# Performance work log

Measured on AMD Instinct MI355X. Metric: run time of the kernel, lower is better.

The kernel has to match this reference:

```python
import jax, jax.numpy as jnp
import numpy as np

L, H, D, DH, DFF, V, P, T, R = 12, 12, 768, 64, 3072, 30522, 512, 2, 50
RAT_LAYER = 6  # original condition: 5 < idx < 7


def layer_norm(x, g, b, eps=1e-12):
    m = x.mean(-1, keepdims=True)
    v = ((x - m) ** 2).mean(-1, keepdims=True)
    return (x - m) / jnp.sqrt(v + eps) * g + b


def setup_inputs() -> dict:
    key = jax.random.key(0)
    ks = iter(jax.random.split(key, 20))
    def n(shape, s=0.02):
        return jax.random.normal(next(ks), shape, dtype=jnp.float32) * s
    inp = dict(
        input_ids=jax.random.randint(next(ks), (4, 512), 0, V, dtype=jnp.int32),
        relations=jax.random.randint(next(ks), (4, 512, 512), 0, R, dtype=jnp.int32),
        attention_mask=jnp.ones((4, 512), dtype=jnp.int32),
        word_emb=n((V, D)), pos_emb=n((P, D)), type_emb=n((T, D)),
        emb_ln_g=jnp.ones((D,)), emb_ln_b=jnp.zeros((D,)),
        Wq=n((L, D, D)), bq=jnp.zeros((L, D)), Wk=n((L, D, D)), bk=jnp.zeros((L, D)),
        Wv=n((L, D, D)), bv=jnp.zeros((L, D)), Wo=n((L, D, D)), bo=jnp.zeros((L, D)),
        ln1_g=jnp.ones((L, D)), ln1_b=jnp.zeros((L, D)),
        Wi=n((L, D, DFF)), bi=jnp.zeros((L, DFF)),
        Wf=n((L, DFF, D)), bf=jnp.zeros((L, D)),
        ln2_g=jnp.ones((L, D)), ln2_b=jnp.zeros((L, D)),
        key_rel=n((L, R, DH)), val_rel=n((L, R, DH)),
        pool_w=n((D, D)), pool_b=jnp.zeros((D,)),
    )
    return inp


def reference(input_ids, relations, attention_mask, word_emb, pos_emb, type_emb,
              emb_ln_g, emb_ln_b, Wq, bq, Wk, bk, Wv, bv, Wo, bo, ln1_g, ln1_b,
              Wi, bi, Wf, bf, ln2_g, ln2_b, key_rel, val_rel, pool_w, pool_b):
    B, S = input_ids.shape
    # BERT embeddings (token_type_ids = zeros as in module default)
    h = word_emb[input_ids] + pos_emb[jnp.arange(S)][None] + type_emb[0][None, None]
    h = layer_norm(h, emb_ln_g, emb_ln_b)
    ext_mask = (1.0 - attention_mask.astype(jnp.float32))[:, None, None, :] * -10000.0
    inv_sqrt_dh = np.float32(1.0 / np.sqrt(DH))
    for i in range(L):
        q = (h @ Wq[i] + bq[i]).reshape(B, S, H, DH).transpose(0, 2, 1, 3)
        k = (h @ Wk[i] + bk[i]).reshape(B, S, H, DH).transpose(0, 2, 1, 3)
        v = (h @ Wv[i] + bv[i]).reshape(B, S, H, DH).transpose(0, 2, 1, 3)
        scores = jnp.einsum('bhsd,bhtd->bhst', q, k)
        if i == RAT_LAYER:
            kr = key_rel[i][relations]            # [B,S,S,DH] gathered relation keys
            scores = scores + jnp.einsum('bhsd,bstd->bhst', q, kr)
        scores = scores * inv_sqrt_dh + ext_mask
        probs = jax.nn.softmax(scores, axis=-1)   # dropout = identity (eval)
        ctx = jnp.einsum('bhst,bhtd->bhsd', probs, v)
        if i == RAT_LAYER:
            vr = val_rel[i][relations]            # [B,S,S,DH] gathered relation values
            ctx = ctx + jnp.einsum('bhst,bstd->bhsd', probs, vr)
        ctx = ctx.transpose(0, 2, 1, 3).reshape(B, S, D)
        attn_out = layer_norm(ctx @ Wo[i] + bo[i] + h, ln1_g[i], ln1_b[i])
        ff = jax.nn.gelu(attn_out @ Wi[i] + bi[i], approximate=False)
        h = layer_norm(ff @ Wf[i] + bf[i] + attn_out, ln2_g[i], ln2_b[i])
    pooled = jnp.tanh(h[:, 0] @ pool_w + pool_b)
    return h, pooled
```

## Files before the change

kernel.cpp:

```cpp
#include <hip/hip_runtime.h>
#include <math.h>

typedef unsigned short u16;
typedef unsigned int   u32;
typedef __bf16  bf16x8 __attribute__((ext_vector_type(8)));
typedef float   f32x4  __attribute__((ext_vector_type(4)));
typedef u16     u16x8  __attribute__((ext_vector_type(8)));

__device__ __forceinline__ u16 f2bf(float f) {
  u32 u = __builtin_bit_cast(u32, f);
  u32 r = (u + 0x7fffu + ((u >> 16) & 1u)) >> 16;
  return (u16)r;
}
__device__ __forceinline__ float bf2f(u16 h) {
  u32 u = ((u32)h) << 16;
  return __builtin_bit_cast(float, u);
}
__device__ __forceinline__ void gload16(const void* g, void* l) {
  __builtin_amdgcn_global_load_lds((const __attribute__((address_space(1))) void*)g,
                                   (__attribute__((address_space(3))) void*)l, 16, 0, 0);
}
__device__ __forceinline__ bf16x8 ld_bf8(const u16* p) {
  u16x8 v = *(const u16x8*)p;
  return __builtin_bit_cast(bf16x8, v);
}
__device__ __forceinline__ f32x4 mfma16(bf16x8 a, bf16x8 b, f32x4 c) {
  return __builtin_amdgcn_mfma_f32_16x16x32_bf16(a, b, c, 0, 0, 0);
}

struct ConvP {
  const float *wq, *wk, *wv, *wo, *wi, *wf;
  u16 *oqkv, *oo, *oi, *of;
};
__global__ __launch_bounds__(256) void conv_weights(ConvP p) {
  int t = blockIdx.x;
  const float* in; u16* out; int K, N, tn, tk;
  if (t < 1728) { int wh = t / 576, tt = t % 576;
    in = wh==0 ? p.wq : (wh==1 ? p.wk : p.wv);
    out = p.oqkv + (size_t)wh * 768 * 768;
    K = 768; N = 768; tn = tt % 24; tk = tt / 24;
  } else if (t < 2304) { int tt = t - 1728; in = p.wo; out = p.oo; K=768;  N=768;  tn=tt%24; tk=tt/24; }
  else if (t < 4608)   { int tt = t - 2304; in = p.wi; out = p.oi; K=768;  N=3072; tn=tt%96; tk=tt/96; }
  else                 { int tt = t - 4608; in = p.wf; out = p.of; K=3072; N=768;  tn=tt%24; tk=tt/24; }
  int n0 = tn*32, k0 = tk*32;
  __shared__ float tile[32][33];
  int x = threadIdx.x, y = threadIdx.y;
  #pragma unroll
  for (int j = 0; j < 4; ++j)
    tile[y + j*8][x] = in[(size_t)(k0 + y + j*8) * N + n0 + x];
  __syncthreads();
  #pragma unroll
  for (int j = 0; j < 4; ++j)
    out[(size_t)(n0 + y + j*8) * K + k0 + x] = f2bf(tile[x][y + j*8]);
}

struct GP {
  const u16* A; const u16* B;
  int K, N;
  long sA, sB, sOut;
  const float* bias; const float* res;
  float* outF; u16* outB;
  const float* bq; const float* bk; const float* bv;
  u16* qO; u16* kO; u16* vO;
};

template<int BM, int BN, int WAVES, int EPI, int KS>
__global__ __launch_bounds__(WAVES*64) void gemm_bt(GP p) {
  constexpr int THREADS = WAVES * 64;
  constexpr int WC = WAVES / 2;
  constexpr int WM = BM / 2, WN = BN / WC, MR = WM / 16, NR = WN / 16;
  constexpr int AIT = BM * 64 / (THREADS * 8);
  constexpr int BIT = BN * 64 / (THREADS * 8);
  const int tid = threadIdx.x;
  const int wave = tid >> 6, lane = tid & 63;
  const int wr = wave / WC, wc = wave % WC;
  const int wm0 = wr * WM, wn0 = wc * WN;
  const int bn = blockIdx.x, bm = blockIdx.y, bz = blockIdx.z;
  const int K = p.K;
  const int kLen = K / KS;
  const int kBeg = (KS > 1) ? bz * kLen : 0;
  const u16* A  = p.A + ((KS > 1) ? 0 : (size_t)bz * p.sA);
  const u16* Bp = p.B + ((KS > 1) ? 0 : (size_t)bz * p.sB);
  const int rowA0 = bm * BM, colB0 = bn * BN;

  __shared__ __align__(16) u16 lds[(BM + BN) * 64];
  u16* Al = lds; u16* Bl = lds + BM * 64;

  f32x4 acc[MR][NR];
  #pragma unroll
  for (int i = 0; i < MR; ++i)
    #pragma unroll
    for (int j = 0; j < NR; ++j) acc[i][j] = f32x4{0.f,0.f,0.f,0.f};

  for (int kt = kBeg; kt < kBeg + kLen; kt += 64) {
    #pragma unroll
    for (int it = 0; it < AIT; ++it) {
      int e = tid * 8 + it * THREADS * 8;
      gload16(A + (size_t)(rowA0 + (e >> 6)) * K + kt + (e & 63), Al + e);
    }
    #pragma unroll
    for (int it = 0; it < BIT; ++it) {
      int e = tid * 8 + it * THREADS * 8;
      gload16(Bp + (size_t)(colB0 + (e >> 6)) * K + kt + (e & 63), Bl + e);
    }
    __syncthreads();
    #pragma unroll
    for (int ks = 0; ks < 2; ++ks) {
      bf16x8 av[MR]; bf16x8 bw[NR];
      #pragma unroll
      for (int mf = 0; mf < MR; ++mf)
        av[mf] = ld_bf8(Al + (wm0 + mf*16 + (lane&15))*64 + ks*32 + (lane>>4)*8);
      #pragma unroll
      for (int nf = 0; nf < NR; ++nf)
        bw[nf] = ld_bf8(Bl + (wn0 + nf*16 + (lane&15))*64 + ks*32 + (lane>>4)*8);
      #pragma unroll
      for (int mf = 0; mf < MR; ++mf)
        #pragma unroll
        for (int nf = 0; nf < NR; ++nf)
          acc[mf][nf] = mfma16(av[mf], bw[nf], acc[mf][nf]);
    }
    __syncthreads();
  }

  #pragma unroll
  for (int mf = 0; mf < MR; ++mf) {
    #pragma unroll
    for (int nf = 0; nf < NR; ++nf) {
      int col = colB0 + wn0 + nf*16 + (lane & 15);
      #pragma unroll
      for (int reg = 0; reg < 4; ++reg) {
        int row = rowA0 + wm0 + mf*16 + (lane >> 4)*4 + reg;
        float v = acc[mf][nf][reg];
        if constexpr (EPI == 0) {
          int wh = col / 768, cc = col % 768;
          int hh = cc >> 6, d = col & 63;
          int b = row >> 9, s = row & 511;
          const float* bias = wh==0 ? p.bq : (wh==1 ? p.bk : p.bv);
          u16 o = f2bf(v + bias[cc]);
          if (wh == 0)      p.qO[((((size_t)b*12 + hh)*512 + s) << 6) + d] = o;
          else if (wh == 1) p.kO[((((size_t)b*12 + hh)*512 + s) << 6) + d] = o;
          else              p.vO[((((size_t)b*12 + hh)*64  + d) << 9) + s] = o;
        } else if constexpr (EPI == 2) {
          p.outF[(size_t)bz * p.sOut + (size_t)row * p.N + col] = v;
        } else {
          float xg = v + p.bias[col];
          float gg = 0.5f * xg * (1.f + erff(xg * 0.70710678118f));
          p.outB[(size_t)row * p.N + col] = f2bf(gg);
        }
      }
    }
  }
}

template<int RAT>
__global__ __launch_bounds__(512) void flash_attn(
    const u16* __restrict__ q, const u16* __restrict__ k, const u16* __restrict__ v,
    const int* __restrict__ mask, u16* __restrict__ ctx,
    const float* __restrict__ qr, const int* __restrict__ rel,
    float* __restrict__ wbins) {
  const int head = blockIdx.x;
  const int bm = blockIdx.y;
  const int b = head / 12, hh = head % 12;
  const int tid = threadIdx.x, wave = tid >> 6, lane = tid & 63;
  const int wr = wave >> 1, wc = wave & 1;
  const int row0 = bm * 64;
  const u16* qb = q + (size_t)head * 512 * 64;
  const u16* kb = k + (size_t)head * 512 * 64;
  const u16* vb = v + (size_t)head * 64 * 512;

  __shared__ __align__(16) u16 Kl[2][64*64];
  __shared__ __align__(16) u16 Vl[2][64*64];
  __shared__ __align__(16) u16 pw[8][16*72];
  __shared__ float em_lds[512];
  __shared__ float mlb[4][16][2];
  __shared__ float qlds[RAT ? 64 : 1][RAT ? 52 : 1];
  __shared__ float wlds[RAT ? 2 : 1][RAT ? 64 : 1][RAT ? 50 : 1];
  __shared__ float scl[RAT ? 2 : 1][RAT ? 64 : 1];
  __shared__ float aex[RAT ? 64 : 1][RAT ? 3 : 1];

  em_lds[tid] = -10000.f * (1.f - (float)mask[b*512 + tid]);
  if constexpr (RAT) {
    for (int i = tid; i < 2*64*50; i += 512) ((float*)wlds)[i] = 0.f;
    for (int i = tid; i < 64*50; i += 512) {
      int rr = i % 50, sr = i / 50;
      qlds[sr][rr] = qr[((size_t)head*512 + row0 + sr)*50 + rr];
    }
  }

  const int qrow = row0 + wr*16 + (lane & 15);
  bf16x8 qf[2];
  qf[0] = ld_bf8(qb + (size_t)qrow*64 +      (lane>>4)*8);
  qf[1] = ld_bf8(qb + (size_t)qrow*64 + 32 + (lane>>4)*8);
  __syncthreads();

  f32x4 ctxacc[4];
  #pragma unroll
  for (int nf = 0; nf < 4; ++nf) ctxacc[nf] = f32x4{0.f,0.f,0.f,0.f};
  float mrun[4], lrun[4];
  #pragma unroll
  for (int r = 0; r < 4; ++r) { mrun[r] = -3.0e38f; lrun[r] = 0.f; }

  const int g = lane >> 4;
  for (int it = 0; it < 4; ++it) {
    {
      int prow = tid >> 3, lcol = (tid & 7) ^ (prow & 7);
      int t0a = it*64, t0b = 256 + it*64;
      gload16(kb + (size_t)(t0a + prow)*64 + lcol*8, Kl[0] + tid*8);
      gload16(kb + (size_t)(t0b + prow)*64 + lcol*8, Kl[1] + tid*8);
      gload16(vb + (size_t)prow*512 + t0a + lcol*8, Vl[0] + tid*8);
      gload16(vb + (size_t)prow*512 + t0b + lcol*8, Vl[1] + tid*8);
    }
    __syncthreads();
    const int tbase = wc*256 + it*64;

    f32x4 s[4];
    #pragma unroll
    for (int nf = 0; nf < 4; ++nf) s[nf] = f32x4{0.f,0.f,0.f,0.f};
    #pragma unroll
    for (int ks = 0; ks < 2; ++ks)
      #pragma unroll
      for (int nf = 0; nf < 4; ++nf) {
        int row = nf*16 + (lane & 15);
        int c16 = (ks*4 + g) ^ (row & 7);
        bf16x8 kf = ld_bf8(Kl[wc] + row*64 + c16*8);
        s[nf] = mfma16(qf[ks], kf, s[nf]);
      }

    u32 rr4[RAT ? 4 : 1];
    if constexpr (RAT) {
      #pragma unroll
      for (int nf = 0; nf < 4; ++nf) {
        int tt = tbase + nf*16 + (lane & 15);
        u32 pack = 0;
        #pragma unroll
        for (int reg = 0; reg < 4; ++reg) {
          int rl = wr*16 + (lane>>4)*4 + reg;
          int rr = rel[((size_t)(b*512 + row0 + rl))*512 + tt];
          pack |= (u32)rr << (8*reg);
          s[nf][reg] += qlds[rl][rr];
        }
        rr4[nf] = pack;
      }
    }

    float em4[4];
    #pragma unroll
    for (int nf = 0; nf < 4; ++nf) em4[nf] = em_lds[tbase + nf*16 + (lane & 15)];

    float scale_[4];
    #pragma unroll
    for (int reg = 0; reg < 4; ++reg) {
      float pm = -3.0e38f;
      #pragma unroll
      for (int nf = 0; nf < 4; ++nf) {
        s[nf][reg] = s[nf][reg]*0.125f + em4[nf];
        pm = fmaxf(pm, s[nf][reg]);
      }
      #pragma unroll
      for (int o = 1; o < 16; o <<= 1) pm = fmaxf(pm, __shfl_xor(pm, o));
      float mnew = fmaxf(mrun[reg], pm);
      float sc = __expf(mrun[reg] - mnew);
      mrun[reg] = mnew;
      scale_[reg] = sc;
      float lsum = 0.f;
      #pragma unroll
      for (int nf = 0; nf < 4; ++nf) {
        float e = __expf(s[nf][reg] - mnew);
        s[nf][reg] = e;
        lsum += e;
      }
      #pragma unroll
      for (int o = 1; o < 16; o <<= 1) lsum += __shfl_xor(lsum, o);
      lrun[reg] = lrun[reg]*sc + lsum;
      if constexpr (RAT) {
        if ((lane & 15) == 0) scl[wc][wr*16 + (lane>>4)*4 + reg] = sc;
      }
    }

    if constexpr (RAT) {
      for (int i = lane; i < 16*50; i += 64) {
        int r = i / 50;
        wlds[wc][wr*16 + r][i % 50] *= scl[wc][wr*16 + r];
      }
      #pragma unroll
      for (int nf = 0; nf < 4; ++nf)
        #pragma unroll
        for (int reg = 0; reg < 4; ++reg) {
          int rl = wr*16 + (lane>>4)*4 + reg;
          int rr = (rr4[nf] >> (8*reg)) & 255;
          atomicAdd(&wlds[wc][rl][rr], s[nf][reg]);
        }
    }

    #pragma unroll
    for (int nf = 0; nf < 4; ++nf)
      #pragma unroll
      for (int reg = 0; reg < 4; ++reg) {
        int qq = (lane>>4)*4 + reg;
        pw[wave][qq*72 + nf*16 + (lane & 15)] = f2bf(s[nf][reg]);
      }

    #pragma unroll
    for (int nf = 0; nf < 4; ++nf)
      #pragma unroll
      for (int reg = 0; reg < 4; ++reg)
        ctxacc[nf][reg] *= scale_[reg];
    #pragma unroll
    for (int ks = 0; ks < 2; ++ks) {
      bf16x8 pf = ld_bf8(pw[wave] + (lane & 15)*72 + ks*32 + g*8);
      #pragma unroll
      for (int nf = 0; nf < 4; ++nf) {
        int row = nf*16 + (lane & 15);
        int c16 = (ks*4 + g) ^ (row & 7);
        bf16x8 vf = ld_bf8(Vl[wc] + row*64 + c16*8);
        ctxacc[nf] = mfma16(pf, vf, ctxacc[nf]);
      }
    }
    __syncthreads();
  }

  float* mergeF = (float*)pw;
  if (wc == 1) {
    #pragma unroll
    for (int nf = 0; nf < 4; ++nf)
      #pragma unroll
      for (int reg = 0; reg < 4; ++reg)
        mergeF[(wr*16 + (lane>>4)*4 + reg)*66 + nf*16 + (lane & 15)] = ctxacc[nf][reg];
    if ((lane & 15) == 0) {
      #pragma unroll
      for (int reg = 0; reg < 4; ++reg) {
        mlb[wr][(lane>>4)*4 + reg][0] = mrun[reg];
        mlb[wr][(lane>>4)*4 + reg][1] = lrun[reg];
      }
    }
  }
  __syncthreads();
  if (wc == 0) {
    float a1[4], a2[4], linv[4];
    #pragma unroll
    for (int reg = 0; reg < 4; ++reg) {
      int r = (lane>>4)*4 + reg;
      float m2 = mlb[wr][r][0], l2 = mlb[wr][r][1];
      float mn = fmaxf(mrun[reg], m2);
      a1[reg] = __expf(mrun[reg] - mn);
      a2[reg] = __expf(m2 - mn);
      linv[reg] = 1.f / (lrun[reg]*a1[reg] + l2*a2[reg]);
      if constexpr (RAT) {
        if ((lane & 15) == 0) {
          aex[wr*16 + r][0] = a1[reg];
          aex[wr*16 + r][1] = a2[reg];
          aex[wr*16 + r][2] = linv[reg];
        }
      }
    }
    #pragma unroll
    for (int nf = 0; nf < 4; ++nf)
      #pragma unroll
      for (int reg = 0; reg < 4; ++reg) {
        int r = wr*16 + (lane>>4)*4 + reg;
        int qg = row0 + r;
        int d = nf*16 + (lane & 15);
        float v2 = mergeF[r*66 + d];
        ctx[((size_t)(b*512 + qg))*768 + hh*64 + d] =
            f2bf((ctxacc[nf][reg]*a1[reg] + v2*a2[reg]) * linv[reg]);
      }
  }
  if constexpr (RAT) {
    __syncthreads();
    for (int i = tid; i < 64*50; i += 512) {
      int sr = i / 50, rr = i % 50;
      wbins[((size_t)head*512 + row0 + sr)*50 + rr] =
          (wlds[0][sr][rr]*aex[sr][0] + wlds[1][sr][rr]*aex[sr][1]) * aex[sr][2];
    }
  }
}

__global__ __launch_bounds__(256) void rat_qr(const u16* __restrict__ q,
    const float* __restrict__ kr, float* __restrict__ qr) {
  int idx = blockIdx.x * 256 + threadIdx.x;
  if (idx >= 24576 * 50) return;
  int r = idx % 50; size_t bhs = (size_t)idx / 50;
  const u16* qp = q + bhs * 64;
  const float* kp = kr + r * 64;
  float acc = 0.f;
  #pragma unroll
  for (int d = 0; d < 64; ++d) acc += bf2f(qp[d]) * kp[d];
  qr[idx] = acc;
}

__global__ __launch_bounds__(256) void rat_apply(const float* __restrict__ wbins,
    const float* __restrict__ vr, u16* __restrict__ ctx) {
  __shared__ float vrl[50*64];
  __shared__ float wl[32*50];
  int tid = threadIdx.x;
  int rows0 = blockIdx.x * 32;
  for (int i = tid; i < 50*64; i += 256) vrl[i] = vr[i];
  for (int i = tid; i < 32*50; i += 256) wl[i] = wbins[(size_t)rows0*50 + i];
  __syncthreads();
  int wave = tid >> 6, lane = tid & 63;
  #pragma unroll
  for (int i = 0; i < 8; ++i) {
    int r = wave*8 + i;
    size_t idx = (size_t)rows0 + r;
    float acc = 0.f;
    #pragma unroll
    for (int j = 0; j < 50; ++j) acc += wl[r*50 + j] * vrl[j*64 + lane];
    int s = (int)(idx & 511); size_t bh = idx >> 9;
    int b = (int)(bh / 12), hh = (int)(bh % 12);
    u16* cp = ctx + ((size_t)(b*512 + s))*768 + hh*64 + lane;
    *cp = f2bf(bf2f(*cp) + acc);
  }
}

__global__ __launch_bounds__(256) void embed_ln(const int* __restrict__ ids,
    const float* __restrict__ we, const float* __restrict__ pe, const float* __restrict__ te,
    const float* __restrict__ g, const float* __restrict__ b,
    float* __restrict__ hF, u16* __restrict__ hB) {
  int row = blockIdx.x, tid = threadIdx.x;
  int s = row & 511;
  int id = ids[row];
  float x[3];
  #pragma unroll
  for (int j = 0; j < 3; ++j) {
    int d = tid + j*256;
    x[j] = we[(size_t)id*768 + d] + pe[(size_t)s*768 + d] + te[d];
  }
  __shared__ float red[4];
  float sm = x[0] + x[1] + x[2];
  #pragma unroll
  for (int o = 32; o; o >>= 1) sm += __shfl_xor(sm, o);
  if (!(tid & 63)) red[tid >> 6] = sm;
  __syncthreads();
  float mean = (red[0]+red[1]+red[2]+red[3]) * (1.f/768.f);
  __syncthreads();
  float q = 0.f;
  #pragma unroll
  for (int j = 0; j < 3; ++j) { float d = x[j] - mean; q += d*d; }
  #pragma unroll
  for (int o = 32; o; o >>= 1) q += __shfl_xor(q, o);
  if (!(tid & 63)) red[tid >> 6] = q;
  __syncthreads();
  float inv = rsqrtf((red[0]+red[1]+red[2]+red[3]) * (1.f/768.f) + 1e-12f);
  #pragma unroll
  for (int j = 0; j < 3; ++j) {
    int d = tid + j*256;
    float y = (x[j] - mean) * inv * g[d] + b[d];
    hF[(size_t)row*768 + d] = y;
    hB[(size_t)row*768 + d] = f2bf(y);
  }
}

__global__ __launch_bounds__(256) void ln_fused(const float* __restrict__ p0,
    const float* __restrict__ p1, const float* __restrict__ p2, const float* __restrict__ p3,
    int np, const float* __restrict__ bias, const float* __restrict__ res,
    const float* __restrict__ g, const float* __restrict__ b,
    float* __restrict__ oF, u16* __restrict__ oB) {
  int row = blockIdx.x, tid = threadIdx.x;
  size_t base = (size_t)row * 768;
  float v[3];
  #pragma unroll
  for (int j = 0; j < 3; ++j) {
    int d = tid + j*256;
    float x = p0[base + d];
    if (np > 1) x += p1[base + d];
    if (np > 2) x += p2[base + d];
    if (np > 3) x += p3[base + d];
    v[j] = x + bias[d] + res[base + d];
  }
  __shared__ float red[4];
  float sm = v[0] + v[1] + v[2];
  #pragma unroll
  for (int o = 32; o; o >>= 1) sm += __shfl_xor(sm, o);
  if (!(tid & 63)) red[tid >> 6] = sm;
  __syncthreads();
  float mean = (red[0]+red[1]+red[2]+red[3]) * (1.f/768.f);
  __syncthreads();
  float q = 0.f;
  #pragma unroll
  for (int j = 0; j < 3; ++j) { float d = v[j] - mean; q += d*d; }
  #pragma unroll
  for (int o = 32; o; o >>= 1) q += __shfl_xor(q, o);
  if (!(tid & 63)) red[tid >> 6] = q;
  __syncthreads();
  float inv = rsqrtf((red[0]+red[1]+red[2]+red[3]) * (1.f/768.f) + 1e-12f);
  #pragma unroll
  for (int j = 0; j < 3; ++j) {
    int d = tid + j*256;
    float y = (v[j] - mean) * inv * g[d] + b[d];
    oF[base + d] = y;
    oB[base + d] = f2bf(y);
  }
}

__global__ __launch_bounds__(256) void pooler_k(const float* __restrict__ h,
    const float* __restrict__ w, const float* __restrict__ bias, float* __restrict__ out) {
  int b = blockIdx.x, tid = threadIdx.x;
  __shared__ float hr[768];
  for (int i = tid; i < 768; i += 256) hr[i] = h[((size_t)b*512)*768 + i];
  __syncthreads();
  float a0 = 0.f, a1 = 0.f, a2 = 0.f;
  for (int kk = 0; kk < 768; ++kk) {
    float hv = hr[kk];
    const float* wr = w + (size_t)kk*768;
    a0 += hv * wr[tid]; a1 += hv * wr[tid+256]; a2 += hv * wr[tid+512];
  }
  out[(size_t)b*768 + tid]       = tanhf(a0 + bias[tid]);
  out[(size_t)b*768 + tid + 256] = tanhf(a1 + bias[tid+256]);
  out[(size_t)b*768 + tid + 512] = tanhf(a2 + bias[tid+512]);
}

__global__ __launch_bounds__(256) void copy_out(const float* __restrict__ in, float* __restrict__ out) {
  size_t i = ((size_t)blockIdx.x * 256 + threadIdx.x) * 4;
  *(float4*)(out + i) = *(const float4*)(in + i);
}

extern "C" void kernel_launch(void* const* d_in, const int* in_sizes, int n_in,
                              void* d_out, int out_size, void* d_ws, size_t ws_size,
                              hipStream_t stream) {
  const int*   ids   = (const int*)d_in[0];
  const int*   rel   = (const int*)d_in[1];
  const int*   amask = (const int*)d_in[2];
  const float* we    = (const float*)d_in[3];
  const float* pe    = (const float*)d_in[4];
  const float* te    = (const float*)d_in[5];
  const float* eg    = (const float*)d_in[6];
  const float* ebb   = (const float*)d_in[7];
  const float* Wq    = (const float*)d_in[8];
  const float* bq    = (const float*)d_in[9];
  const float* Wk    = (const float*)d_in[10];
  const float* bk    = (const float*)d_in[11];
  const float* Wv    = (const float*)d_in[12];
  const float* bv    = (const float*)d_in[13];
  const float* Wo    = (const float*)d_in[14];
  const float* bo    = (const float*)d_in[15];
  const float* g1    = (const float*)d_in[16];
  const float* b1    = (const float*)d_in[17];
  const float* Wi    = (const float*)d_in[18];
  const float* bi    = (const float*)d_in[19];
  const float* Wf    = (const float*)d_in[20];
  const float* bfp   = (const float*)d_in[21];
  const float* g2    = (const float*)d_in[22];
  const float* b2    = (const float*)d_in[23];
  const float* krel  = (const float*)d_in[24];
  const float* vrel  = (const float*)d_in[25];
  const float* pwp   = (const float*)d_in[26];
  const float* pbp   = (const float*)d_in[27];
  (void)in_sizes; (void)n_in; (void)out_size; (void)ws_size;

  char* ws = (char*)d_ws;
  size_t off = 0;
  auto take = [&](size_t bytes) { char* p = ws + off; off += (bytes + 255) & ~(size_t)255; return p; };
  u16*   wqkv = (u16*)take((size_t)2304*768*2);
  u16*   wo_l = (u16*)take((size_t)768*768*2);
  u16*   wi_l = (u16*)take((size_t)3072*768*2);
  u16*   wf_l = (u16*)take((size_t)768*3072*2);
  float* hF   = (float*)take((size_t)2048*768*4);
  u16*   hB   = (u16*)take((size_t)2048*768*2);
  float* atF  = (float*)take((size_t)2048*768*4);
  u16*   atB  = (u16*)take((size_t)2048*768*2);
  u16*   qB   = (u16*)take((size_t)2048*768*2);
  u16*   kB   = (u16*)take((size_t)2048*768*2);
  u16*   vB   = (u16*)take((size_t)2048*768*2);
  u16*   ctxB = (u16*)take((size_t)2048*768*2);
  float* tmpF = (float*)take((size_t)4*2048*768*4);
  u16*   ffB  = (u16*)take((size_t)2048*3072*2);
  float* qrF  = (float*)take((size_t)24576*50*4);
  float* wbF  = (float*)take((size_t)24576*50*4);
  const size_t PSTRIDE = (size_t)2048*768;

  embed_ln<<<2048, 256, 0, stream>>>(ids, we, pe, te, eg, ebb, hF, hB);

  for (int l = 0; l < 12; ++l) {
    ConvP cp{Wq + (size_t)l*768*768, Wk + (size_t)l*768*768, Wv + (size_t)l*768*768,
             Wo + (size_t)l*768*768, Wi + (size_t)l*768*3072, Wf + (size_t)l*3072*768,
             wqkv, wo_l, wi_l, wf_l};
    conv_weights<<<6912, dim3(32,8), 0, stream>>>(cp);

    GP pq{}; pq.A = hB; pq.B = wqkv; pq.K = 768; pq.N = 2304;
    pq.bq = bq + l*768; pq.bk = bk + l*768; pq.bv = bv + l*768;
    pq.qO = qB; pq.kO = kB; pq.vO = vB;
    gemm_bt<128,128,8,0,1><<<dim3(18,16,1), 512, 0, stream>>>(pq);

    if (l == 6) {
      rat_qr<<<4800, 256, 0, stream>>>(qB, krel + 6*50*64, qrF);
      flash_attn<1><<<dim3(48,8), 512, 0, stream>>>(qB, kB, vB, amask, ctxB, qrF, rel, wbF);
      rat_apply<<<768, 256, 0, stream>>>(wbF, vrel + 6*50*64, ctxB);
    } else {
      flash_attn<0><<<dim3(48,8), 512, 0, stream>>>(qB, kB, vB, amask, ctxB, nullptr, nullptr, nullptr);
    }

    GP po{}; po.A = ctxB; po.B = wo_l; po.K = 768; po.N = 768; po.sOut = PSTRIDE;
    po.outF = tmpF;
    gemm_bt<64,128,4,2,2><<<dim3(6,32,2), 256, 0, stream>>>(po);
    ln_fused<<<2048, 256, 0, stream>>>(tmpF, tmpF + PSTRIDE, nullptr, nullptr, 2,
                                       bo + l*768, hF, g1 + l*768, b1 + l*768, atF, atB);

    GP pf1{}; pf1.A = atB; pf1.B = wi_l; pf1.K = 768; pf1.N = 3072;
    pf1.bias = bi + (size_t)l*3072; pf1.outB = ffB;
    gemm_bt<128,128,8,3,1><<<dim3(24,16,1), 512, 0, stream>>>(pf1);

    GP pf2{}; pf2.A = ffB; pf2.B = wf_l; pf2.K = 3072; pf2.N = 768; pf2.sOut = PSTRIDE;
    pf2.outF = tmpF;
    gemm_bt<64,128,4,2,4><<<dim3(6,32,4), 256, 0, stream>>>(pf2);
    ln_fused<<<2048, 256, 0, stream>>>(tmpF, tmpF + PSTRIDE, tmpF + 2*PSTRIDE, tmpF + 3*PSTRIDE, 4,
                                       bfp + l*768, atF, g2 + l*768, b2 + l*768, hF, hB);
  }

  copy_out<<<1536, 256, 0, stream>>>(hF, (float*)d_out);
  pooler_k<<<4, 256, 0, stream>>>(hF, pwp, pbp, (float*)d_out + (size_t)2048*768);
}
```

Measured before the change: 1.888 ms.

## Batch all-layer weight conversion into one launch and halve attention query tiles

When the workspace is large enough, weight fp32-to-bf16 transposition for all 12 layers is done in a single up-front launch instead of one per layer, removing 11 launches and their serialization with the GEMMs. Flash attention now uses 32-row query tiles with 256 threads and twice as many blocks, which raises block count and occupancy at the cost of loading K/V tiles twice as often. It needs more workspace memory for per-layer weight copies and falls back to the per-layer path otherwise.

```diff
diff --git a/kernel.cpp b/kernel.cpp
--- a/kernel.cpp
+++ b/kernel.cpp
@@ -31,17 +31,26 @@
 struct ConvP {
   const float *wq, *wk, *wv, *wo, *wi, *wf;
   u16 *oqkv, *oo, *oi, *of;
+  long doqkv, doo, doi, dof;
 };
-__global__ __launch_bounds__(256) void conv_weights(ConvP p) {
-  int t = blockIdx.x;
+__global__ __launch_bounds__(256) void conv_weights(ConvP p, int l0) {
+  int l = l0 + blockIdx.x / 6912;
+  int t = blockIdx.x % 6912;
   const float* in; u16* out; int K, N, tn, tk;
   if (t < 1728) { int wh = t / 576, tt = t % 576;
-    in = wh==0 ? p.wq : (wh==1 ? p.wk : p.wv);
-    out = p.oqkv + (size_t)wh * 768 * 768;
+    in = (wh==0 ? p.wq : (wh==1 ? p.wk : p.wv)) + (size_t)l*768*768;
+    out = p.oqkv + (size_t)l*p.doqkv + (size_t)wh * 768 * 768;
     K = 768; N = 768; tn = tt % 24; tk = tt / 24;
-  } else if (t < 2304) { int tt = t - 1728; in = p.wo; out = p.oo; K=768;  N=768;  tn=tt%24; tk=tt/24; }
-  else if (t < 4608)   { int tt = t - 2304; in = p.wi; out = p.oi; K=768;  N=3072; tn=tt%96; tk=tt/96; }
-  else                 { int tt = t - 4608; in = p.wf; out = p.of; K=3072; N=768;  tn=tt%24; tk=tt/24; }
+  } else if (t < 2304) { int tt = t - 1728;
+    in = p.wo + (size_t)l*768*768; out = p.oo + (size_t)l*p.doo;
+    K=768;  N=768;  tn=tt%24; tk=tt/24;
+  } else if (t < 4608) { int tt = t - 2304;
+    in = p.wi + (size_t)l*768*3072; out = p.oi + (size_t)l*p.doi;
+    K=768;  N=3072; tn=tt%96; tk=tt/96;
+  } else { int tt = t - 4608;
+    in = p.wf + (size_t)l*768*3072; out = p.of + (size_t)l*p.dof;
+    K=3072; N=768;  tn=tt%24; tk=tt/24;
+  }
   int n0 = tn*32, k0 = tk*32;
   __shared__ float tile[32][33];
   int x = threadIdx.x, y = threadIdx.y;
@@ -153,7 +162,7 @@
 }
 
 template<int RAT>
-__global__ __launch_bounds__(512) void flash_attn(
+__global__ __launch_bounds__(256) void flash_attn(
     const u16* __restrict__ q, const u16* __restrict__ k, const u16* __restrict__ v,
     const int* __restrict__ mask, u16* __restrict__ ctx,
     const float* __restrict__ qr, const int* __restrict__ rel,
@@ -163,25 +172,26 @@
   const int b = head / 12, hh = head % 12;
   const int tid = threadIdx.x, wave = tid >> 6, lane = tid & 63;
   const int wr = wave >> 1, wc = wave & 1;
-  const int row0 = bm * 64;
+  const int row0 = bm * 32;
   const u16* qb = q + (size_t)head * 512 * 64;
   const u16* kb = k + (size_t)head * 512 * 64;
   const u16* vb = v + (size_t)head * 64 * 512;
 
   __shared__ __align__(16) u16 Kl[2][64*64];
   __shared__ __align__(16) u16 Vl[2][64*64];
-  __shared__ __align__(16) u16 pw[8][16*72];
+  __shared__ __align__(16) u16 pw[4][16*72];
   __shared__ float em_lds[512];
-  __shared__ float mlb[4][16][2];
-  __shared__ float qlds[RAT ? 64 : 1][RAT ? 52 : 1];
-  __shared__ float wlds[RAT ? 2 : 1][RAT ? 64 : 1][RAT ? 50 : 1];
-  __shared__ float scl[RAT ? 2 : 1][RAT ? 64 : 1];
-  __shared__ float aex[RAT ? 64 : 1][RAT ? 3 : 1];
-
-  em_lds[tid] = -10000.f * (1.f - (float)mask[b*512 + tid]);
+  __shared__ float mlb[2][16][2];
+  __shared__ float qlds[RAT ? 32 : 1][RAT ? 52 : 1];
+  __shared__ float wlds[RAT ? 2 : 1][RAT ? 32 : 1][RAT ? 50 : 1];
+  __shared__ float scl[RAT ? 2 : 1][RAT ? 32 : 1];
+  __shared__ float aex[RAT ? 32 : 1][RAT ? 3 : 1];
+
+  for (int i = tid; i < 512; i += 256)
+    em_lds[i] = -10000.f * (1.f - (float)mask[b*512 + i]);
   if constexpr (RAT) {
-    for (int i = tid; i < 2*64*50; i += 512) ((float*)wlds)[i] = 0.f;
-    for (int i = tid; i < 64*50; i += 512) {
+    for (int i = tid; i < 2*32*50; i += 256) ((float*)wlds)[i] = 0.f;
+    for (int i = tid; i < 32*50; i += 256) {
       int rr = i % 50, sr = i / 50;
       qlds[sr][rr] = qr[((size_t)head*512 + row0 + sr)*50 + rr];
     }
@@ -202,13 +212,15 @@
 
   const int g = lane >> 4;
   for (int it = 0; it < 4; ++it) {
-    {
-      int prow = tid >> 3, lcol = (tid & 7) ^ (prow & 7);
+    #pragma unroll
+    for (int j = 0; j < 2; ++j) {
+      int s = j*256 + tid;
+      int prow = s >> 3, c16 = (s & 7) ^ (prow & 7);
       int t0a = it*64, t0b = 256 + it*64;
-      gload16(kb + (size_t)(t0a + prow)*64 + lcol*8, Kl[0] + tid*8);
-      gload16(kb + (size_t)(t0b + prow)*64 + lcol*8, Kl[1] + tid*8);
-      gload16(vb + (size_t)prow*512 + t0a + lcol*8, Vl[0] + tid*8);
-      gload16(vb + (size_t)prow*512 + t0b + lcol*8, Vl[1] + tid*8);
+      gload16(kb + (size_t)(t0a + prow)*64 + c16*8, Kl[0] + s*8);
+      gload16(kb + (size_t)(t0b + prow)*64 + c16*8, Kl[1] + s*8);
+      gload16(vb + (size_t)prow*512 + t0a + c16*8, Vl[0] + s*8);
+      gload16(vb + (size_t)prow*512 + t0b + c16*8, Vl[1] + s*8);
     }
     __syncthreads();
     const int tbase = wc*256 + it*64;
@@ -367,7 +379,7 @@
   }
   if constexpr (RAT) {
     __syncthreads();
-    for (int i = tid; i < 64*50; i += 512) {
+    for (int i = tid; i < 32*50; i += 256) {
       int sr = i / 50, rr = i % 50;
       wbins[((size_t)head*512 + row0 + sr)*50 + rr] =
           (wlds[0][sr][rr]*aex[sr][0] + wlds[1][sr][rr]*aex[sr][1]) * aex[sr][2];
@@ -545,15 +557,11 @@
   const float* vrel  = (const float*)d_in[25];
   const float* pwp   = (const float*)d_in[26];
   const float* pbp   = (const float*)d_in[27];
-  (void)in_sizes; (void)n_in; (void)out_size; (void)ws_size;
+  (void)in_sizes; (void)n_in; (void)out_size;
 
   char* ws = (char*)d_ws;
   size_t off = 0;
   auto take = [&](size_t bytes) { char* p = ws + off; off += (bytes + 255) & ~(size_t)255; return p; };
-  u16*   wqkv = (u16*)take((size_t)2304*768*2);
-  u16*   wo_l = (u16*)take((size_t)768*768*2);
-  u16*   wi_l = (u16*)take((size_t)3072*768*2);
-  u16*   wf_l = (u16*)take((size_t)768*3072*2);
   float* hF   = (float*)take((size_t)2048*768*4);
   u16*   hB   = (u16*)take((size_t)2048*768*2);
   float* atF  = (float*)take((size_t)2048*768*4);
@@ -568,25 +576,41 @@
   float* wbF  = (float*)take((size_t)24576*50*4);
   const size_t PSTRIDE = (size_t)2048*768;
 
+  const size_t WQKV = (size_t)2304*768, WWO = (size_t)768*768;
+  const size_t WWI = (size_t)768*3072, WWF = (size_t)3072*768;
+  const size_t wLayerBytes = (WQKV + WWO + WWI + WWF) * 2;
+  const bool preall = (off + 12*wLayerBytes + 65536 <= ws_size);
+  const int NL = preall ? 12 : 1;
+  u16* wqkvB = (u16*)take(WQKV*2*NL);
+  u16* woB   = (u16*)take(WWO*2*NL);
+  u16* wiB   = (u16*)take(WWI*2*NL);
+  u16* wfB   = (u16*)take(WWF*2*NL);
+
+  ConvP cp{Wq, Wk, Wv, Wo, Wi, Wf, wqkvB, woB, wiB, wfB,
+           preall ? (long)WQKV : 0, preall ? (long)WWO : 0,
+           preall ? (long)WWI : 0, preall ? (long)WWF : 0};
+
   embed_ln<<<2048, 256, 0, stream>>>(ids, we, pe, te, eg, ebb, hF, hB);
+  if (preall) conv_weights<<<12*6912, dim3(32,8), 0, stream>>>(cp, 0);
 
   for (int l = 0; l < 12; ++l) {
-    ConvP cp{Wq + (size_t)l*768*768, Wk + (size_t)l*768*768, Wv + (size_t)l*768*768,
-             Wo + (size_t)l*768*768, Wi + (size_t)l*768*3072, Wf + (size_t)l*3072*768,
-             wqkv, wo_l, wi_l, wf_l};
-    conv_weights<<<6912, dim3(32,8), 0, stream>>>(cp);
-
-    GP pq{}; pq.A = hB; pq.B = wqkv; pq.K = 768; pq.N = 2304;
+    if (!preall) conv_weights<<<6912, dim3(32,8), 0, stream>>>(cp, l);
+    const u16* wqkv_l = wqkvB + (size_t)l*cp.doqkv;
+    const u16* wo_l   = woB   + (size_t)l*cp.doo;
+    const u16* wi_l   = wiB   + (size_t)l*cp.doi;
+    const u16* wf_l   = wfB   + (size_t)l*cp.dof;
+
+    GP pq{}; pq.A = hB; pq.B = wqkv_l; pq.K = 768; pq.N = 2304;
     pq.bq = bq + l*768; pq.bk = bk + l*768; pq.bv = bv + l*768;
     pq.qO = qB; pq.kO = kB; pq.vO = vB;
     gemm_bt<128,128,8,0,1><<<dim3(18,16,1), 512, 0, stream>>>(pq);
 
     if (l == 6) {
       rat_qr<<<4800, 256, 0, stream>>>(qB, krel + 6*50*64, qrF);
-      flash_attn<1><<<dim3(48,8), 512, 0, stream>>>(qB, kB, vB, amask, ctxB, qrF, rel, wbF);
+      flash_attn<1><<<dim3(48,16), 256, 0, stream>>>(qB, kB, vB, amask, ctxB, qrF, rel, wbF);
       rat_apply<<<768, 256, 0, stream>>>(wbF, vrel + 6*50*64, ctxB);
     } else {
-      flash_attn<0><<<dim3(48,8), 512, 0, stream>>>(qB, kB, vB, amask, ctxB, nullptr, nullptr, nullptr);
+      flash_attn<0><<<dim3(48,16), 256, 0, stream>>>(qB, kB, vB, amask, ctxB, nullptr, nullptr, nullptr);
     }
 
     GP po{}; po.A = ctxB; po.B = wo_l; po.K = 768; po.N = 768; po.sOut = PSTRIDE;
```

Result: no change. 1.884 ms (-0.2%).
